# Kernel optimization log

Measured on AMD Instinct MI355X. Metric: run time of the kernel, lower is better.

The kernel has to match this reference:

```python
import jax, jax.numpy as jnp
import numpy as np


def setup_inputs() -> dict:
    key = jax.random.key(0)
    ks = jax.random.split(key, 6)
    N, F, D, K, B = 100000, 128, 64, 128, 16384
    X = jax.random.normal(ks[0], (N, F), dtype=jnp.float32)
    idx = jax.random.randint(ks[1], (B,), 0, N, dtype=jnp.int64)
    indices = jax.random.randint(ks[2], (N, K), 0, N, dtype=jnp.int64)
    values = jax.random.uniform(ks[3], (N, K), dtype=jnp.float32)
    W = jax.random.normal(ks[4], (F, D), dtype=jnp.float32) * 0.02
    b = jnp.zeros((D,), dtype=jnp.float32)
    return {"X": X, "idx": idx, "indices": indices, "values": values, "W": W, "b": b}


def reference(X, idx, indices, values, W, b):
    # Sparse branch of _PPR.forward:
    #   ind = indices[idx]; val = values[idx]
    #   out = (encoder(X[unique])[inverse] * val[..., None]).sum(axis=1)
    # unique/inverse is a dedup optimization; math is identical to encoding
    # all nodes once and gathering (jit-friendly, no dynamic shapes).
    enc = X @ W + b                       # [N, D]  encoder(X)
    nbr = indices[idx]                    # [B, K]  topk-PPR neighbor ids per seed
    val = values[idx]                     # [B, K]  PPR weights
    gathered = enc[nbr]                   # [B, K, D]
    return (gathered * val[..., None]).sum(axis=1)  # [B, D]
```

## Files before the change

### kernel.cpp

```cpp
#include <hip/hip_runtime.h>

#define F_DIM 128
#define D_DIM 64
#define K_NBR 128

typedef _Float16 half8 __attribute__((ext_vector_type(8)));
typedef _Float16 half4 __attribute__((ext_vector_type(4)));
typedef float f32x4 __attribute__((ext_vector_type(4)));

#define XPAD 8
#define LDK (F_DIM + XPAD)

__global__ __launch_bounds__(256) void encode_mfma(
    const float* __restrict__ X, const float* __restrict__ W,
    const float* __restrict__ bias, _Float16* __restrict__ enc, int n)
{
    __shared__ _Float16 WT[D_DIM][LDK];
    __shared__ _Float16 Xs[64][LDK];
    __shared__ float    bs[D_DIM];

    const int t = threadIdx.x;

    #pragma unroll
    for (int i = 0; i < (F_DIM * D_DIM) / 256; ++i) {
        int lin = i * 256 + t;
        int f = lin >> 6, d = lin & 63;
        WT[d][f] = (_Float16)W[lin];
    }
    if (t < D_DIM) bs[t] = bias[t];

    const int w    = t >> 6;
    const int l    = t & 63;
    const int lrow = l & 15;
    const int lgrp = l >> 4;

    __syncthreads();

    half8 bfr[4][4];
    #pragma unroll
    for (int ct = 0; ct < 4; ++ct)
        #pragma unroll
        for (int kk = 0; kk < 4; ++kk)
            bfr[ct][kk] = *reinterpret_cast<const half8*>(
                &WT[ct * 16 + lrow][kk * 32 + lgrp * 8]);

    const int rowbase0 = blockIdx.x * 256;

    for (int tile = 0; tile < 4; ++tile) {
        const int rb = rowbase0 + tile * 64;
        __syncthreads();
        #pragma unroll
        for (int i = 0; i < 8; ++i) {
            int lin4 = i * 256 + t;
            int row  = lin4 >> 5;
            int k4   = lin4 & 31;
            int sr   = rb + row; if (sr >= n) sr = n - 1;
            float4 x = reinterpret_cast<const float4*>(X)[(size_t)sr * 32 + k4];
            half4 h;
            h.x = (_Float16)x.x; h.y = (_Float16)x.y;
            h.z = (_Float16)x.z; h.w = (_Float16)x.w;
            *reinterpret_cast<half4*>(&Xs[row][k4 * 4]) = h;
        }
        __syncthreads();

        f32x4 acc[4] = {{0.f,0.f,0.f,0.f},{0.f,0.f,0.f,0.f},
                        {0.f,0.f,0.f,0.f},{0.f,0.f,0.f,0.f}};
        #pragma unroll
        for (int kk = 0; kk < 4; ++kk) {
            half8 a = *reinterpret_cast<const half8*>(
                &Xs[w * 16 + lrow][kk * 32 + lgrp * 8]);
            #pragma unroll
            for (int ct = 0; ct < 4; ++ct)
                acc[ct] = __builtin_amdgcn_mfma_f32_16x16x32_f16(
                    a, bfr[ct][kk], acc[ct], 0, 0, 0);
        }

        #pragma unroll
        for (int r = 0; r < 4; ++r) {
            int row = rb + w * 16 + lgrp * 4 + r;
            if (row < n) {
                #pragma unroll
                for (int ct = 0; ct < 4; ++ct) {
                    enc[(size_t)row * D_DIM + ct * 16 + lrow] =
                        (_Float16)(acc[ct][r] + bs[ct * 16 + lrow]);
                }
            }
        }
    }
}

__global__ __launch_bounds__(256) void gather_wide(
    const int* __restrict__ idx, const int* __restrict__ indices,
    const float* __restrict__ values, const _Float16* __restrict__ enc,
    float* __restrict__ out)
{
    __shared__ int   ids[K_NBR];
    __shared__ float vs[K_NBR];
    __shared__ float partial[4][D_DIM];

    const int b = blockIdx.x;
    const int t = threadIdx.x;

    const int sid = idx[b];
    if (t < K_NBR) {
        ids[t] = indices[(size_t)sid * K_NBR + t];
        vs[t]  = values[(size_t)sid * K_NBR + t];
    }
    __syncthreads();

    const int w    = t >> 6;
    const int l    = t & 63;
    const int rsub = l >> 3;
    const int dblk = l & 7;

    float acc[8] = {0.f,0.f,0.f,0.f,0.f,0.f,0.f,0.f};

    #pragma unroll
    for (int it = 0; it < 4; ++it) {
        const int   k  = w * 32 + it * 8 + rsub;
        const int   id = ids[k];
        const float v  = vs[k];
        half8 h = *reinterpret_cast<const half8*>(
            enc + (size_t)id * D_DIM + dblk * 8);
        #pragma unroll
        for (int j = 0; j < 8; ++j)
            acc[j] += v * (float)h[j];
    }

    #pragma unroll
    for (int m = 8; m < 64; m <<= 1) {
        #pragma unroll
        for (int j = 0; j < 8; ++j)
            acc[j] += __shfl_xor(acc[j], m, 64);
    }

    if (l < 8) {
        #pragma unroll
        for (int j = 0; j < 8; ++j)
            partial[w][l * 8 + j] = acc[j];
    }
    __syncthreads();

    if (w == 0) {
        out[(size_t)b * D_DIM + l] =
            partial[0][l] + partial[1][l] + partial[2][l] + partial[3][l];
    }
}

extern "C" void kernel_launch(void* const* d_in, const int* in_sizes, int n_in,
                              void* d_out, int out_size, void* d_ws, size_t ws_size,
                              hipStream_t stream) {
    const float* X       = (const float*)d_in[0];
    const int*   idx     = (const int*)d_in[1];
    const int*   indices = (const int*)d_in[2];
    const float* values  = (const float*)d_in[3];
    const float* W       = (const float*)d_in[4];
    const float* bias    = (const float*)d_in[5];
    float*       out     = (float*)d_out;

    const int N = in_sizes[0] / F_DIM;
    const int B = in_sizes[1];

    _Float16* enc = (_Float16*)d_ws;

    const int grid1 = (N + 255) / 256;
    encode_mfma<<<grid1, 256, 0, stream>>>(X, W, bias, enc, N);

    gather_wide<<<B, 256, 0, stream>>>(idx, indices, values, enc, out);
}
```

Measured before the change: 52.68 us.

## Sort neighbor gathers by id bucket and process 8 seeds per block

The gather kernel now handles 8 seeds per block instead of one. It counting-sorts each seed's 128 neighbors into 16 id-range buckets in shared memory and then walks the sorted list in lockstep phases with block-wide barriers, so concurrent waves touch nearby regions of the encoded table. The aim is better L2/MALL locality on the random gathers and less per-block setup. It also software-pipelines the enc loads and writes outputs with vector stores. In exchange it adds atomics, a serial prefix scan by one thread, and extra barriers inside the loop.

```diff
diff --git a/kernel.cpp b/kernel.cpp
--- a/kernel.cpp
+++ b/kernel.cpp
@@ -3,6 +3,10 @@
 #define F_DIM 128
 #define D_DIM 64
 #define K_NBR 128
+#define SPB   8
+#define NBKT  16
+#define NKEY  (SPB * NBKT)
+#define NPHASE 4
 
 typedef _Float16 half8 __attribute__((ext_vector_type(8)));
 typedef _Float16 half4 __attribute__((ext_vector_type(4)));
@@ -89,22 +93,49 @@
     }
 }
 
-__global__ __launch_bounds__(256) void gather_wide(
+__global__ __launch_bounds__(256, 8) void gather_sorted(
     const int* __restrict__ idx, const int* __restrict__ indices,
     const float* __restrict__ values, const _Float16* __restrict__ enc,
-    float* __restrict__ out)
+    float* __restrict__ out, int B, float inv_bsz)
 {
-    __shared__ int   ids[K_NBR];
-    __shared__ float vs[K_NBR];
-    __shared__ float partial[4][D_DIM];
-
-    const int b = blockIdx.x;
-    const int t = threadIdx.x;
-
-    const int sid = idx[b];
-    if (t < K_NBR) {
-        ids[t] = indices[(size_t)sid * K_NBR + t];
-        vs[t]  = values[(size_t)sid * K_NBR + t];
+    __shared__ int  cnt[NKEY];
+    __shared__ int  base[NKEY];
+    __shared__ int2 spair[SPB * K_NBR];
+
+    const int t  = threadIdx.x;
+    const int b0 = blockIdx.x * SPB;
+
+    if (t < NKEY) cnt[t] = 0;
+    __syncthreads();
+
+    int eid[4]; float ev[4]; int ekey[4]; int erank[4];
+    #pragma unroll
+    for (int i = 0; i < 4; ++i) {
+        int e = i * 256 + t;
+        int s = e >> 7;
+        int j = e & 127;
+        int seed = b0 + s; if (seed >= B) seed = B - 1;
+        int srow = idx[seed];
+        eid[i] = indices[(size_t)srow * K_NBR + j];
+        ev[i]  = values[(size_t)srow * K_NBR + j];
+        int bkt = (int)((float)eid[i] * inv_bsz);
+        if (bkt > NBKT - 1) bkt = NBKT - 1;
+        ekey[i] = (s << 4) | bkt;
+        erank[i] = atomicAdd(&cnt[ekey[i]], 1);
+    }
+    __syncthreads();
+
+    if (t == 0) {
+        int run = 0;
+        #pragma unroll 4
+        for (int k = 0; k < NKEY; ++k) { base[k] = run; run += cnt[k]; }
+    }
+    __syncthreads();
+
+    #pragma unroll
+    for (int i = 0; i < 4; ++i) {
+        int dst = base[ekey[i]] + erank[i];
+        spair[dst] = make_int2(eid[i], __float_as_int(ev[i]));
     }
     __syncthreads();
 
@@ -112,38 +143,67 @@
     const int l    = t & 63;
     const int rsub = l >> 3;
     const int dblk = l & 7;
-
-    float acc[8] = {0.f,0.f,0.f,0.f,0.f,0.f,0.f,0.f};
-
-    #pragma unroll
-    for (int it = 0; it < 4; ++it) {
-        const int   k  = w * 32 + it * 8 + rsub;
-        const int   id = ids[k];
-        const float v  = vs[k];
-        half8 h = *reinterpret_cast<const half8*>(
-            enc + (size_t)id * D_DIM + dblk * 8);
-        #pragma unroll
-        for (int j = 0; j < 8; ++j)
-            acc[j] += v * (float)h[j];
+    const int sA   = 2 * w;
+    const int sB   = 2 * w + 1;
+
+    float accA[8] = {0,0,0,0,0,0,0,0};
+    float accB[8] = {0,0,0,0,0,0,0,0};
+
+    for (int p = 0; p < NPHASE; ++p) {
+        const int kb = p * 32 + rsub;
+        int2 pa = spair[sA * K_NBR + kb];
+        int2 pb = spair[sB * K_NBR + kb];
+        half8 hA = *reinterpret_cast<const half8*>(
+            enc + (size_t)pa.x * D_DIM + dblk * 8);
+        half8 hB = *reinterpret_cast<const half8*>(
+            enc + (size_t)pb.x * D_DIM + dblk * 8);
+        float vA = __int_as_float(pa.y), vB = __int_as_float(pb.y);
+
+        #pragma unroll
+        for (int c = 0; c < 4; ++c) {
+            half8 nA, nB; float nvA, nvB;
+            if (c < 3) {
+                int2 na = spair[sA * K_NBR + kb + (c + 1) * 8];
+                int2 nb = spair[sB * K_NBR + kb + (c + 1) * 8];
+                nA = *reinterpret_cast<const half8*>(
+                    enc + (size_t)na.x * D_DIM + dblk * 8);
+                nB = *reinterpret_cast<const half8*>(
+                    enc + (size_t)nb.x * D_DIM + dblk * 8);
+                nvA = __int_as_float(na.y); nvB = __int_as_float(nb.y);
+            }
+            #pragma unroll
+            for (int j = 0; j < 8; ++j) {
+                accA[j] += vA * (float)hA[j];
+                accB[j] += vB * (float)hB[j];
+            }
+            if (c < 3) { hA = nA; hB = nB; vA = nvA; vB = nvB; }
+        }
+        __syncthreads();
     }
 
     #pragma unroll
     for (int m = 8; m < 64; m <<= 1) {
         #pragma unroll
-        for (int j = 0; j < 8; ++j)
-            acc[j] += __shfl_xor(acc[j], m, 64);
+        for (int j = 0; j < 8; ++j) {
+            accA[j] += __shfl_xor(accA[j], m, 64);
+            accB[j] += __shfl_xor(accB[j], m, 64);
+        }
     }
 
     if (l < 8) {
-        #pragma unroll
-        for (int j = 0; j < 8; ++j)
-            partial[w][l * 8 + j] = acc[j];
-    }
-    __syncthreads();
-
-    if (w == 0) {
-        out[(size_t)b * D_DIM + l] =
-            partial[0][l] + partial[1][l] + partial[2][l] + partial[3][l];
+        const int gA = b0 + sA, gB = b0 + sB;
+        if (gA < B) {
+            float4 o0 = make_float4(accA[0], accA[1], accA[2], accA[3]);
+            float4 o1 = make_float4(accA[4], accA[5], accA[6], accA[7]);
+            reinterpret_cast<float4*>(out + (size_t)gA * D_DIM + l * 8)[0] = o0;
+            reinterpret_cast<float4*>(out + (size_t)gA * D_DIM + l * 8)[1] = o1;
+        }
+        if (gB < B) {
+            float4 o0 = make_float4(accB[0], accB[1], accB[2], accB[3]);
+            float4 o1 = make_float4(accB[4], accB[5], accB[6], accB[7]);
+            reinterpret_cast<float4*>(out + (size_t)gB * D_DIM + l * 8)[0] = o0;
+            reinterpret_cast<float4*>(out + (size_t)gB * D_DIM + l * 8)[1] = o1;
+        }
     }
 }
 
@@ -166,5 +226,9 @@
     const int grid1 = (N + 255) / 256;
     encode_mfma<<<grid1, 256, 0, stream>>>(X, W, bias, enc, N);
 
-    gather_wide<<<B, 256, 0, stream>>>(idx, indices, values, enc, out);
+    const int   bucket_sz = (N + NBKT - 1) / NBKT;
+    const float inv_bsz   = 1.0f / (float)bucket_sz;
+    const int   grid2     = (B + SPB - 1) / SPB;
+    gather_sorted<<<grid2, 256, 0, stream>>>(idx, indices, values, enc, out,
+                                             B, inv_bsz);
 }
```

After: 54.51 us. 1.03x slower.
